# Performance work log

Measured on AMD Instinct MI355X. Metric: run time of the kernel, lower is better.

## Reference

```python
import jax, jax.numpy as jnp
import numpy as np

B, S, D, H, E = 4, 2048, 256, 8, 65536
HD = D // H  # head_dim = 32


def _layernorm(x, g, b, eps=1e-5):
    mu = jnp.mean(x, axis=-1, keepdims=True)
    var = jnp.var(x, axis=-1, keepdims=True)
    return (x - mu) * jax.lax.rsqrt(var + eps) * g + b


def setup_inputs() -> dict:
    key = jax.random.key(0)
    ks = jax.random.split(key, 16)
    sd = 1.0 / np.sqrt(D)
    inp = {
        "x": jax.random.normal(ks[0], (B, S, D), jnp.float32),
        "adj_mask": jax.random.uniform(ks[1], (B, S, S)) < 0.05,  # ~32 neighbors/node
        "edge_attr": jax.random.normal(ks[2], (E,), jnp.float32),
        "edge_index": jax.random.randint(ks[3], (2, E), 0, S),
        "ln1_g": jnp.ones((D,), jnp.float32),
        "ln1_b": jnp.zeros((D,), jnp.float32),
        "wq": jax.random.normal(ks[4], (D, D), jnp.float32) * sd,
        "bq": jnp.zeros((D,), jnp.float32),
        "wk": jax.random.normal(ks[5], (D, D), jnp.float32) * sd,
        "bk": jnp.zeros((D,), jnp.float32),
        "wv": jax.random.normal(ks[6], (D, D), jnp.float32) * sd,
        "bv": jnp.zeros((D,), jnp.float32),
        "wo": jax.random.normal(ks[7], (D, D), jnp.float32) * sd,
        "bo": jnp.zeros((D,), jnp.float32),
        "ln2_g": jnp.ones((D,), jnp.float32),
        "ln2_b": jnp.zeros((D,), jnp.float32),
        "w1": jax.random.normal(ks[8], (4 * D, D), jnp.float32) * sd,
        "b1": jnp.zeros((4 * D,), jnp.float32),
        "w2": jax.random.normal(ks[9], (D, 4 * D), jnp.float32) * (1.0 / np.sqrt(4 * D)),
        "b2": jnp.zeros((D,), jnp.float32),
    }
    return inp


def reference(x, adj_mask, edge_attr, edge_index,
              ln1_g, ln1_b, wq, bq, wk, bk, wv, bv, wo, bo,
              ln2_g, ln2_b, w1, b1, w2, b2):
    residual = x
    nx = _layernorm(x, ln1_g, ln1_b)
    # projections (torch Linear: y = x W^T + b)
    q = nx @ wq.T + bq
    k = nx @ wk.T + bk
    v = nx @ wv.T + bv
    # (B,S,D) -> (B,H,S,HD)
    q = q.reshape(B, S, H, HD).transpose(0, 2, 1, 3)
    k = k.reshape(B, S, H, HD).transpose(0, 2, 1, 3)
    v = v.reshape(B, S, H, HD).transpose(0, 2, 1, 3)
    scores = jnp.einsum("bhqd,bhkd->bhqk", q, k) / np.sqrt(HD)
    scores = jnp.where(adj_mask[:, None, :, :], scores, -1e9)
    # edge-attr bias: scatter clipped attr into (S,S), gated per-batch by adj_mask,
    # broadcast over heads (replaces the nested python loop)
    clipped = jnp.clip(edge_attr, -5.0, 5.0)
    bias2d = jnp.zeros((S, S), scores.dtype).at[edge_index[0], edge_index[1]].set(clipped)
    scores = scores + jnp.where(adj_mask, bias2d[None, :, :], 0.0)[:, None, :, :]
    attn = jax.nn.softmax(scores, axis=-1)
    ctx = jnp.einsum("bhqk,bhkd->bhqd", attn, v)
    ctx = ctx.transpose(0, 2, 1, 3).reshape(B, S, D)
    x = residual + (ctx @ wo.T + bo)
    # MLP block (exact GELU, like torch nn.GELU())
    n2 = _layernorm(x, ln2_g, ln2_b)
    h = jax.nn.gelu(n2 @ w1.T + b1, approximate=False)
    x = x + (h @ w2.T + b2)
    return x
```

## Files before the change

### kernel.cpp

```cpp
#include <hip/hip_runtime.h>
#include <stdint.h>

#define S 2048
#define D 256
#define H 8
#define HD 32
#define E_EDGES 65536
#define DFF 1024
#define M_TOK 8192
#define CAP 512
#define QKVN 768

typedef __attribute__((ext_vector_type(8))) short s16x8;
typedef __attribute__((ext_vector_type(8))) unsigned short u16x8;
typedef __attribute__((ext_vector_type(4))) unsigned short u16x4v;
typedef __attribute__((ext_vector_type(4))) float f32x4;

__device__ __forceinline__ float b2f(unsigned short u){
  union { unsigned int i; float f; } x; x.i = ((unsigned int)u) << 16; return x.f;
}
__device__ __forceinline__ unsigned short f2b(float f){
  union { float f; unsigned int i; } x; x.f = f;
  unsigned int r = x.i + 0x7fffu + ((x.i >> 16) & 1u);
  return (unsigned short)(r >> 16);
}
__device__ __forceinline__ void gload_lds16(const void* g, void* l) {
  __builtin_amdgcn_global_load_lds(
      (const __attribute__((address_space(1))) unsigned int*)g,
      (__attribute__((address_space(3))) unsigned int*)l, 16, 0, 0);
}

__global__ __launch_bounds__(256) void prep_kernel(
    const float* __restrict__ wq, const float* __restrict__ wk,
    const float* __restrict__ wv, const float* __restrict__ wo,
    const float* __restrict__ w1, const float* __restrict__ w2,
    unsigned short* __restrict__ wqkvb, unsigned short* __restrict__ wob,
    unsigned short* __restrict__ w1b, unsigned short* __restrict__ w2b)
{
  const int i = blockIdx.x * 256 + threadIdx.x;
  const float* src; unsigned short* dst; int off;
  if      (i <  16384) { src = wq; dst = wqkvb;            off = i; }
  else if (i <  32768) { src = wk; dst = wqkvb +  65536;   off = i -  16384; }
  else if (i <  49152) { src = wv; dst = wqkvb + 131072;   off = i -  32768; }
  else if (i <  65536) { src = wo; dst = wob;              off = i -  49152; }
  else if (i < 131072) { src = w1; dst = w1b;              off = i -  65536; }
  else                 { src = w2; dst = w2b;              off = i - 131072; }
  const float4 v = ((const float4*)src)[off];
  unsigned short o[4] = { f2b(v.x), f2b(v.y), f2b(v.z), f2b(v.w) };
  *(uint2*)(dst + (size_t)off * 4) = *(const uint2*)o;
}

__global__ __launch_bounds__(192) void bias_kernel(
    const float* __restrict__ bq, const float* __restrict__ bk,
    const float* __restrict__ bv, float* __restrict__ bqkv)
{
  const int i = threadIdx.x;
  if      (i <  64) ((float4*)bqkv)[i] = ((const float4*)bq)[i];
  else if (i < 128) ((float4*)bqkv)[i] = ((const float4*)bk)[i - 64];
  else              ((float4*)bqkv)[i] = ((const float4*)bv)[i - 128];
}

__global__ __launch_bounds__(256) void ln_kernel(
    const float* __restrict__ xf,
    const float* __restrict__ g, const float* __restrict__ bt,
    unsigned short* __restrict__ out)
{
  const int wave = threadIdx.x >> 6;
  const int lane = threadIdx.x & 63;
  const int row = blockIdx.x * 4 + wave;
  const size_t base = (size_t)row * D + lane * 4;
  const float4 u = *(const float4*)(xf + base);
  float v[4] = { u.x, u.y, u.z, u.w };
  float s  = v[0]+v[1]+v[2]+v[3];
  float s2 = v[0]*v[0]+v[1]*v[1]+v[2]*v[2]+v[3]*v[3];
  #pragma unroll
  for (int off=32; off>=1; off>>=1){ s += __shfl_xor(s,off,64); s2 += __shfl_xor(s2,off,64); }
  const float mu  = s * (1.f/D);
  const float var = s2 * (1.f/D) - mu*mu;
  const float rs  = 1.f / sqrtf(var + 1e-5f);
  #pragma unroll
  for (int j=0;j<4;++j){
    const int c = lane*4 + j;
    const float y = (v[j]-mu)*rs*g[c] + bt[c];
    out[(size_t)row*D + c] = f2b(y);
  }
}

template<int BM, int BN, int WR, int WC>
__global__ __launch_bounds__(256) void gemm_lds(
    const unsigned short* __restrict__ A,
    const unsigned short* __restrict__ W,
    const float* __restrict__ bias,
    unsigned short* __restrict__ outb,
    float* __restrict__ outf,
    const float* __restrict__ resf,
    int M, int N, int K, int act)
{
  constexpr int WM = BM / WR, WN = BN / WC;
  constexpr int MI = WM / 16, NI = WN / 16;
  __shared__ unsigned short As[2][BM * 32];
  __shared__ unsigned short Bs[2][BN * 32];
  const int tid  = threadIdx.x;
  const int wave = tid >> 6;
  const int lane = tid & 63;
  const int wr = wave / WC, wc = wave % WC;
  const int m0 = blockIdx.y * BM;
  const int n0 = blockIdx.x * BN;
  const int ldr = lane >> 2;
  const int ldc = (lane & 3) * 8;
  const int fr = lane & 15;
  const int kf = (lane >> 4) * 8;
  f32x4 acc[MI][NI];
  #pragma unroll
  for (int i=0;i<MI;++i)
    #pragma unroll
    for (int j=0;j<NI;++j)
      #pragma unroll
      for (int r=0;r<4;++r) acc[i][j][r] = 0.f;

  auto stage = [&](int buf, int k0) {
    #pragma unroll
    for (int c = wave; c < BM/16; c += 4)
      gload_lds16(A + (size_t)(m0 + c*16 + ldr)*K + k0 + ldc, &As[buf][c*512]);
    #pragma unroll
    for (int c = wave; c < BN/16; c += 4)
      gload_lds16(W + (size_t)(n0 + c*16 + ldr)*K + k0 + ldc, &Bs[buf][c*512]);
  };

  stage(0, 0);
  __syncthreads();
  int cur = 0;
  for (int k0 = 0; k0 < K; k0 += 32) {
    if (k0 + 32 < K) stage(cur ^ 1, k0 + 32);
    s16x8 af[MI], bf[NI];
    #pragma unroll
    for (int i = 0; i < MI; ++i) af[i] = *(const s16x8*)&As[cur][(wr*WM + i*16 + fr)*32 + kf];
    #pragma unroll
    for (int j = 0; j < NI; ++j) bf[j] = *(const s16x8*)&Bs[cur][(wc*WN + j*16 + fr)*32 + kf];
    #pragma unroll
    for (int i = 0; i < MI; ++i)
      #pragma unroll
      for (int j = 0; j < NI; ++j)
        acc[i][j] = __builtin_amdgcn_mfma_f32_16x16x32_bf16(af[i], bf[j], acc[i][j], 0, 0, 0);
    __syncthreads();
    cur ^= 1;
  }
  const int rbase = (lane >> 4) * 4;
  #pragma unroll
  for (int j = 0; j < NI; ++j) {
    const int col = n0 + wc*WN + j*16 + fr;
    const float bvl = bias[col];
    #pragma unroll
    for (int i = 0; i < MI; ++i) {
      #pragma unroll
      for (int r = 0; r < 4; ++r) {
        const int row = m0 + wr*WM + i*16 + rbase + r;
        const size_t off = (size_t)row * N + col;
        float vv = acc[i][j][r] + bvl;
        if (act) vv = 0.5f * vv * (1.0f + erff(vv * 0.70710678118654752f));
        if (resf) vv += resf[off];
        if (outb) outb[off] = f2b(vv);
        if (outf) outf[off] = vv;
      }
    }
  }
}

__global__ __launch_bounds__(256) void zero_kernel(uint4* __restrict__ p, int n4) {
  int i = blockIdx.x * 256 + threadIdx.x;
  if (i < n4) { uint4 z; z.x=0; z.y=0; z.z=0; z.w=0; p[i] = z; }
}
__global__ __launch_bounds__(256) void scatter_kernel(
    const int* __restrict__ ei, const float* __restrict__ attr,
    unsigned int* __restrict__ packed)
{
  int e = blockIdx.x * 256 + threadIdx.x;
  if (e >= E_EDGES) return;
  int r = ei[e], c = ei[E_EDGES + e];
  float v = attr[e];
  v = fminf(5.f, fmaxf(-5.f, v));
  unsigned int pk = (((unsigned int)e) << 16) | (unsigned int)f2b(v);
  atomicMax(&packed[(size_t)r * S + c], pk);
}

__global__ __launch_bounds__(256) void attn_kernel(
    const unsigned short* __restrict__ qkv,
    const int* __restrict__ mask,
    const unsigned int* __restrict__ packed,
    unsigned short* __restrict__ ctx)
{
  __shared__ unsigned short nidx[CAP];
  __shared__ unsigned int noff[CAP];
  __shared__ float nbias[CAP];
  __shared__ float sc[CAP*9];
  __shared__ float red[4*D];
  __shared__ float rsum[H];
  __shared__ int wtot[4], wbase[4], cnt_s;
  const int t = threadIdx.x;
  const int wave = t >> 6, lane = t & 63;
  const int bqi = blockIdx.x;
  const int b = bqi >> 11;
  const int qrow = bqi & (S-1);

  const int* mrow = mask + (size_t)bqi * S;
  const uint4 ma = *(const uint4*)(mrow + t*8);
  const uint4 mb = *(const uint4*)(mrow + t*8 + 4);
  unsigned int mv[8] = { ma.x, ma.y, ma.z, ma.w, mb.x, mb.y, mb.z, mb.w };
  int mycnt = 0;
  #pragma unroll
  for (int j = 0; j < 8; ++j) mycnt += mv[j] ? 1 : 0;
  int inc = mycnt;
  #pragma unroll
  for (int off=1; off<64; off<<=1){ int y = __shfl_up(inc, off, 64); if (lane >= off) inc += y; }
  if (lane == 63) wtot[wave] = inc;
  __syncthreads();
  if (t == 0) { int ss=0; for (int w=0; w<4; ++w){ wbase[w]=ss; ss+=wtot[w]; } cnt_s = ss; }
  __syncthreads();
  int pos = wbase[wave] + inc - mycnt;
  #pragma unroll
  for (int j = 0; j < 8; ++j) {
    if (mv[j]) {
      if (pos < CAP) nidx[pos] = (unsigned short)(t*8 + j);
      ++pos;
    }
  }
  __syncthreads();
  int cnt = cnt_s; if (cnt > CAP) cnt = CAP;
  const int cnt_pad = (cnt + 31) & ~31;
  for (int i = cnt + t; i < cnt_pad; i += 256) { nidx[i] = 0; noff[i] = 512u; nbias[i] = 0.f; }

  for (int i = t; i < cnt; i += 256) {
    const unsigned int ni = nidx[i];
    noff[i] = ni * 1536u + 512u;
    unsigned int pkv = packed[(size_t)qrow * S + ni];
    nbias[i] = b2f((unsigned short)(pkv & 0xffffu));
  }
  __syncthreads();

  const int ns = lane >> 3;
  const int hh = lane & 7;
  const float scale = 0.17677669529663687f;
  const char* kbase = (const char*)(qkv + (size_t)b * S * QKVN) + hh * 64;

  float q32[32];
  {
    const u16x8* qp = (const u16x8*)(qkv + (size_t)bqi * QKVN + hh * HD);
    #pragma unroll
    for (int c = 0; c < 4; ++c) {
      u16x8 qv = qp[c];
      #pragma unroll
      for (int j = 0; j < 8; ++j) q32[c*8+j] = b2f(qv[j]);
    }
  }

  for (int n0 = wave*8; n0 < cnt_pad; n0 += 32) {
    const int n = n0 + ns;
    const unsigned int off = noff[n];
    const u16x8* kp = (const u16x8*)(kbase + off);
    u16x8 kv0 = kp[0], kv1 = kp[1], kv2 = kp[2], kv3 = kp[3];
    float d0 = 0.f, d1 = 0.f, d2 = 0.f, d3 = 0.f;
    #pragma unroll
    for (int j = 0; j < 8; ++j) {
      d0 += q32[j]    * b2f(kv0[j]);
      d1 += q32[8+j]  * b2f(kv1[j]);
      d2 += q32[16+j] * b2f(kv2[j]);
      d3 += q32[24+j] * b2f(kv3[j]);
    }
    const float scv = ((d0+d1)+(d2+d3)) * scale + nbias[n];
    sc[n*9 + hh] = (n < cnt) ? scv : 0.f;
  }
  __syncthreads();

  if (cnt > 0) {
    const int h = t >> 5, dd = t & 31;
    float m = -1e30f;
    for (int n = dd; n < cnt; n += 32) m = fmaxf(m, sc[n*9 + h]);
    #pragma unroll
    for (int off=16; off>=1; off>>=1) m = fmaxf(m, __shfl_xor(m, off, 64));
    float sum = 0.f;
    for (int n = dd; n < cnt; n += 32) {
      float e = __expf(sc[n*9 + h] - m);
      sc[n*9 + h] = e;
      sum += e;
    }
    #pragma unroll
    for (int off=16; off>=1; off>>=1) sum += __shfl_xor(sum, off, 64);
    if (dd == 0) rsum[h] = 1.f / sum;
  }
  __syncthreads();

  if (cnt > 0) {
    float a32[32];
    #pragma unroll
    for (int j = 0; j < 32; ++j) a32[j] = 0.f;
    for (int n0 = wave*8; n0 < cnt_pad; n0 += 32) {
      const int n = n0 + ns;
      const unsigned int off = noff[n];
      const u16x8* vp = (const u16x8*)(kbase + off + 512);
      u16x8 v0 = vp[0], v1 = vp[1], v2 = vp[2], v3 = vp[3];
      const float p = sc[n*9 + hh];
      #pragma unroll
      for (int j = 0; j < 8; ++j) {
        a32[j]    += p * b2f(v0[j]);
        a32[8+j]  += p * b2f(v1[j]);
        a32[16+j] += p * b2f(v2[j]);
        a32[24+j] += p * b2f(v3[j]);
      }
    }
    #pragma unroll
    for (int mm = 8; mm <= 32; mm <<= 1)
      #pragma unroll
      for (int j = 0; j < 32; ++j) a32[j] += __shfl_xor(a32[j], mm, 64);
    if (ns == 0) {
      #pragma unroll
      for (int c = 0; c < 8; ++c) {
        f32x4 w4 = { a32[c*4], a32[c*4+1], a32[c*4+2], a32[c*4+3] };
        *(f32x4*)&red[wave*D + hh*HD + c*4] = w4;
      }
    }
  } else {
    float a4[4] = {0.f, 0.f, 0.f, 0.f};
    for (int n = wave; n < S; n += 4) {
      const u16x4v vv = *(const u16x4v*)((const char*)(qkv + (size_t)b*S*QKVN) + (size_t)n*1536 + 1024 + lane*8);
      a4[0] += b2f(vv[0]); a4[1] += b2f(vv[1]); a4[2] += b2f(vv[2]); a4[3] += b2f(vv[3]);
    }
    #pragma unroll
    for (int j = 0; j < 4; ++j) a4[j] *= (1.f / S);
    *(f32x4*)&red[wave*D + lane*4] = *(f32x4*)a4;
    if (t < 8) rsum[t] = 1.f;
  }
  __syncthreads();
  const float outv = (red[t] + red[D + t] + red[2*D + t] + red[3*D + t]) * rsum[t >> 5];
  ctx[(size_t)bqi * D + t] = f2b(outv);
}

extern "C" void kernel_launch(void* const* d_in, const int* in_sizes, int n_in,
                              void* d_out, int out_size, void* d_ws, size_t ws_size,
                              hipStream_t stream) {
  const float*          x    = (const float*)d_in[0];
  const int*            mask = (const int*)d_in[1];
  const float*          eat  = (const float*)d_in[2];
  const int*            eidx = (const int*)d_in[3];
  const float*          ln1g = (const float*)d_in[4];
  const float*          ln1b = (const float*)d_in[5];
  const float*          wq   = (const float*)d_in[6];
  const float*          bq   = (const float*)d_in[7];
  const float*          wk   = (const float*)d_in[8];
  const float*          bk   = (const float*)d_in[9];
  const float*          wv   = (const float*)d_in[10];
  const float*          bv   = (const float*)d_in[11];
  const float*          wo   = (const float*)d_in[12];
  const float*          bo   = (const float*)d_in[13];
  const float*          ln2g = (const float*)d_in[14];
  const float*          ln2b = (const float*)d_in[15];
  const float*          w1   = (const float*)d_in[16];
  const float*          b1   = (const float*)d_in[17];
  const float*          w2   = (const float*)d_in[18];
  const float*          b2   = (const float*)d_in[19];
  float* out = (float*)d_out;

  char* ws = (char*)d_ws;
  unsigned short* nx   = (unsigned short*)ws;
  unsigned short* qkv  = nx + (size_t)M_TOK*D;
  unsigned short* cx   = qkv + (size_t)M_TOK*QKVN;
  float*          x1   = (float*)(cx + (size_t)M_TOK*D);
  unsigned int*   pk   = (unsigned int*)(x1 + (size_t)M_TOK*D);
  unsigned short* wqkvb= (unsigned short*)(pk + (size_t)S*S);
  unsigned short* wob  = wqkvb + (size_t)QKVN*D;
  unsigned short* w1b  = wob + (size_t)D*D;
  unsigned short* w2b  = w1b + (size_t)DFF*D;
  float*          bqkv = (float*)(w2b + (size_t)D*DFF);
  unsigned short* hb   = qkv;
  unsigned short* n2   = nx;

  prep_kernel<<<768, 256, 0, stream>>>(wq, wk, wv, wo, w1, w2, wqkvb, wob, w1b, w2b);
  bias_kernel<<<1, 192, 0, stream>>>(bq, bk, bv, bqkv);
  zero_kernel<<<(S*S/4 + 255)/256, 256, 0, stream>>>((uint4*)pk, S*S/4);
  scatter_kernel<<<E_EDGES/256, 256, 0, stream>>>(eidx, eat, pk);
  ln_kernel<<<M_TOK/4, 256, 0, stream>>>(x, ln1g, ln1b, nx);
  gemm_lds<64,128,1,4><<<dim3(QKVN/128, M_TOK/64), 256, 0, stream>>>(nx, wqkvb, bqkv, qkv, nullptr, nullptr, M_TOK, QKVN, D, 0);
  attn_kernel<<<M_TOK, 256, 0, stream>>>(qkv, mask, pk, cx);
  gemm_lds<64,64,2,2><<<dim3(D/64, M_TOK/64), 256, 0, stream>>>(cx, wob, bo, nullptr, x1, x, M_TOK, D, D, 0);
  ln_kernel<<<M_TOK/4, 256, 0, stream>>>(x1, ln2g, ln2b, n2);
  gemm_lds<128,128,2,2><<<dim3(DFF/128, M_TOK/128), 256, 0, stream>>>(n2, w1b, b1, hb, nullptr, nullptr, M_TOK, DFF, D, 1);
  gemm_lds<64,64,2,2><<<dim3(D/64, M_TOK/64), 256, 0, stream>>>(hb, w2b, b2, nullptr, out, x1, M_TOK, D, DFF, 0);
}
```

Before: 187.2 us.

## Compute neighbor attention scores with MFMA over LDS-staged K and restructure PV

Gathered K rows for each chunk of 64 neighbors are staged into LDS with swizzled global_load_lds. The QK dot products are then computed with 16x16x32 bf16 MFMA, using a block-diagonal query fragment so that each output column holds one head. The PV accumulation is rewritten so each lane owns 4 output dims and reads V coalesced across 8 neighbors, which removes the 32-register accumulator and its cross-lane shuffle reduction. CAP is reduced to 256, which shrinks shared memory. The cost is an extra sync per chunk and possible truncation of unusually dense rows.

```diff
diff --git a/kernel.cpp b/kernel.cpp
--- a/kernel.cpp
+++ b/kernel.cpp
@@ -8,7 +8,8 @@
 #define E_EDGES 65536
 #define DFF 1024
 #define M_TOK 8192
-#define CAP 512
+#define CAP 256
+#define CHUNK 64
 #define QKVN 768
 
 typedef __attribute__((ext_vector_type(8))) short s16x8;
@@ -18,6 +19,12 @@
 
 __device__ __forceinline__ float b2f(unsigned short u){
   union { unsigned int i; float f; } x; x.i = ((unsigned int)u) << 16; return x.f;
+}
+__device__ __forceinline__ float u2f_lo(unsigned int u){
+  union { unsigned int i; float f; } x; x.i = u << 16; return x.f;
+}
+__device__ __forceinline__ float u2f_hi(unsigned int u){
+  union { unsigned int i; float f; } x; x.i = u & 0xffff0000u; return x.f;
 }
 __device__ __forceinline__ unsigned short f2b(float f){
   union { float f; unsigned int i; } x; x.f = f;
@@ -189,6 +196,7 @@
     const unsigned int* __restrict__ packed,
     unsigned short* __restrict__ ctx)
 {
+  __shared__ unsigned short K_lds[CHUNK*256];
   __shared__ unsigned short nidx[CAP];
   __shared__ unsigned int noff[CAP];
   __shared__ float nbias[CAP];
@@ -201,6 +209,7 @@
   const int bqi = blockIdx.x;
   const int b = bqi >> 11;
   const int qrow = bqi & (S-1);
+  const char* qkvb = (const char*)(qkv + (size_t)b * S * QKVN);
 
   const int* mrow = mask + (size_t)bqi * S;
   const uint4 ma = *(const uint4*)(mrow + t*8);
@@ -226,9 +235,8 @@
   }
   __syncthreads();
   int cnt = cnt_s; if (cnt > CAP) cnt = CAP;
-  const int cnt_pad = (cnt + 31) & ~31;
+  const int cnt_pad = (cnt + (CHUNK-1)) & ~(CHUNK-1);
   for (int i = cnt + t; i < cnt_pad; i += 256) { nidx[i] = 0; noff[i] = 512u; nbias[i] = 0.f; }
-
   for (int i = t; i < cnt; i += 256) {
     const unsigned int ni = nidx[i];
     noff[i] = ni * 1536u + 512u;
@@ -237,39 +245,40 @@
   }
   __syncthreads();
 
-  const int ns = lane >> 3;
-  const int hh = lane & 7;
+  const int fr = lane & 15;
+  const int kq = lane >> 4;
   const float scale = 0.17677669529663687f;
-  const char* kbase = (const char*)(qkv + (size_t)b * S * QKVN) + hh * 64;
-
-  float q32[32];
-  {
-    const u16x8* qp = (const u16x8*)(qkv + (size_t)bqi * QKVN + hh * HD);
-    #pragma unroll
-    for (int c = 0; c < 4; ++c) {
-      u16x8 qv = qp[c];
-      #pragma unroll
-      for (int j = 0; j < 8; ++j) q32[c*8+j] = b2f(qv[j]);
-    }
-  }
-
-  for (int n0 = wave*8; n0 < cnt_pad; n0 += 32) {
-    const int n = n0 + ns;
-    const unsigned int off = noff[n];
-    const u16x8* kp = (const u16x8*)(kbase + off);
-    u16x8 kv0 = kp[0], kv1 = kp[1], kv2 = kp[2], kv3 = kp[3];
-    float d0 = 0.f, d1 = 0.f, d2 = 0.f, d3 = 0.f;
-    #pragma unroll
-    for (int j = 0; j < 8; ++j) {
-      d0 += q32[j]    * b2f(kv0[j]);
-      d1 += q32[8+j]  * b2f(kv1[j]);
-      d2 += q32[16+j] * b2f(kv2[j]);
-      d3 += q32[24+j] * b2f(kv3[j]);
-    }
-    const float scv = ((d0+d1)+(d2+d3)) * scale + nbias[n];
-    sc[n*9 + hh] = (n < cnt) ? scv : 0.f;
-  }
-  __syncthreads();
+
+  s16x8 qfrag = *(const s16x8*)(qkv + (size_t)bqi * QKVN + fr*HD + kq*8);
+  const s16x8 zfrag = {0,0,0,0,0,0,0,0};
+  s16x8 bf8[8];
+  #pragma unroll
+  for (int kk = 0; kk < 8; ++kk) bf8[kk] = (fr == kk) ? qfrag : zfrag;
+
+  for (int c0 = 0; c0 < cnt_pad; c0 += CHUNK) {
+    #pragma unroll
+    for (int ii = 0; ii < 8; ++ii) {
+      const int s = wave*16 + 2*ii + (lane >> 5);
+      const unsigned int go = noff[c0 + s] + ((unsigned)((lane & 31) ^ (s & 7)) << 4);
+      gload_lds16(qkvb + go, &K_lds[(wave*16 + 2*ii)*256]);
+    }
+    __syncthreads();
+    f32x4 acc = {0.f, 0.f, 0.f, 0.f};
+    #pragma unroll
+    for (int kk = 0; kk < 8; ++kk) {
+      const int cidx = (kk*4 + kq) ^ (lane & 7);
+      s16x8 af = *(const s16x8*)&K_lds[(wave*16 + fr)*256 + cidx*8];
+      acc = __builtin_amdgcn_mfma_f32_16x16x32_bf16(af, bf8[kk], acc, 0, 0, 0);
+    }
+    if (fr < 8) {
+      #pragma unroll
+      for (int r = 0; r < 4; ++r) {
+        const int n = c0 + wave*16 + kq*4 + r;
+        sc[n*9 + fr] = (n < cnt) ? acc[r]*scale + nbias[n] : 0.f;
+      }
+    }
+    __syncthreads();
+  }
 
   if (cnt > 0) {
     const int h = t >> 5, dd = t & 31;
@@ -289,46 +298,34 @@
   }
   __syncthreads();
 
+  const int hh = lane >> 3;
+  float a4[4] = {0.f, 0.f, 0.f, 0.f};
   if (cnt > 0) {
-    float a32[32];
-    #pragma unroll
-    for (int j = 0; j < 32; ++j) a32[j] = 0.f;
     for (int n0 = wave*8; n0 < cnt_pad; n0 += 32) {
-      const int n = n0 + ns;
-      const unsigned int off = noff[n];
-      const u16x8* vp = (const u16x8*)(kbase + off + 512);
-      u16x8 v0 = vp[0], v1 = vp[1], v2 = vp[2], v3 = vp[3];
-      const float p = sc[n*9 + hh];
-      #pragma unroll
-      for (int j = 0; j < 8; ++j) {
-        a32[j]    += p * b2f(v0[j]);
-        a32[8+j]  += p * b2f(v1[j]);
-        a32[16+j] += p * b2f(v2[j]);
-        a32[24+j] += p * b2f(v3[j]);
+      uint2 vv[8];
+      #pragma unroll
+      for (int u = 0; u < 8; ++u)
+        vv[u] = *(const uint2*)(qkvb + noff[n0+u] + 512 + lane*8);
+      #pragma unroll
+      for (int u = 0; u < 8; ++u) {
+        const float p = sc[(n0+u)*9 + hh];
+        a4[0] += p * u2f_lo(vv[u].x);
+        a4[1] += p * u2f_hi(vv[u].x);
+        a4[2] += p * u2f_lo(vv[u].y);
+        a4[3] += p * u2f_hi(vv[u].y);
       }
     }
-    #pragma unroll
-    for (int mm = 8; mm <= 32; mm <<= 1)
-      #pragma unroll
-      for (int j = 0; j < 32; ++j) a32[j] += __shfl_xor(a32[j], mm, 64);
-    if (ns == 0) {
-      #pragma unroll
-      for (int c = 0; c < 8; ++c) {
-        f32x4 w4 = { a32[c*4], a32[c*4+1], a32[c*4+2], a32[c*4+3] };
-        *(f32x4*)&red[wave*D + hh*HD + c*4] = w4;
-      }
-    }
   } else {
-    float a4[4] = {0.f, 0.f, 0.f, 0.f};
     for (int n = wave; n < S; n += 4) {
-      const u16x4v vv = *(const u16x4v*)((const char*)(qkv + (size_t)b*S*QKVN) + (size_t)n*1536 + 1024 + lane*8);
-      a4[0] += b2f(vv[0]); a4[1] += b2f(vv[1]); a4[2] += b2f(vv[2]); a4[3] += b2f(vv[3]);
+      const uint2 vv = *(const uint2*)(qkvb + (size_t)n*1536 + 1024 + lane*8);
+      a4[0] += u2f_lo(vv.x); a4[1] += u2f_hi(vv.x);
+      a4[2] += u2f_lo(vv.y); a4[3] += u2f_hi(vv.y);
     }
     #pragma unroll
     for (int j = 0; j < 4; ++j) a4[j] *= (1.f / S);
-    *(f32x4*)&red[wave*D + lane*4] = *(f32x4*)a4;
     if (t < 8) rsum[t] = 1.f;
   }
+  *(f32x4*)&red[wave*D + lane*4] = *(f32x4*)a4;
   __syncthreads();
   const float outv = (red[t] + red[D + t] + red[2*D + t] + red[3*D + t]) * rsum[t >> 5];
   ctx[(size_t)bqi * D + t] = f2b(outv);
```

After: 187.0 us. Within noise of the previous version (-0.1%).
